# Performance work log

Measured on AMD Instinct MI355X. Metric: run time of the kernel, lower is better.

## Reference

```python
import jax, jax.numpy as jnp
import numpy as np

SPARSE_DEGREE = 4   # MUL_LEV_SPA_ATN_SPARSE_DEGREES[level=1]
NUM_HEADS = 16


def setup_inputs() -> dict:
    key = jax.random.key(0)
    k1, k2, k3 = jax.random.split(key, 3)
    S, B, H, Dh = 4096, 2, NUM_HEADS, 128  # [seq, batch, heads, head_dim]
    q = jax.random.normal(k1, (S, B, H, Dh), jnp.float32)
    k = jax.random.normal(k2, (S, B, H, Dh), jnp.float32)
    v = jax.random.normal(k3, (S, B, H, Dh), jnp.float32)
    return {"q": q, "k": k, "v": v}


def reference(q, k, v):
    # Single-device (world_size=1) MLSAForOneLevel forward, is_prompt=True.
    d = SPARSE_DEGREE
    S, B, H, Dh = q.shape
    Ssp = S // d  # number of sparse tokens per head

    # Per-head strided indices: head h selects tokens h%d, h%d+d, ...  -> [Ssp, H]
    idx = (jnp.arange(H) % d)[None, :] + d * jnp.arange(Ssp)[:, None]
    idx4 = jnp.broadcast_to(idx[:, None, :, None], (Ssp, B, H, Dh))
    gather0 = lambda x: jnp.take_along_axis(x, idx4, axis=0)
    q_ = gather0(q)  # prompt phase: q is also sparsified
    k_ = gather0(k)
    v_ = gather0(v)

    # Core attention (causal), layout [t, b, h, d]
    scale = 1.0 / jnp.sqrt(jnp.asarray(Dh, q.dtype))
    scores = jnp.einsum('tbhd,sbhd->bhts', q_, k_) * scale  # [B,H,Ssp,Ssp]
    causal = jnp.tril(jnp.ones((Ssp, Ssp), bool))
    scores = jnp.where(causal[None, None], scores, -jnp.inf)
    m = jnp.max(scores, axis=-1, keepdims=True)
    e = jnp.exp(scores - m)
    denom = jnp.sum(e, axis=-1, keepdims=True)          # softmax denominator [B,H,Ssp,1]
    probs = e / denom
    ctx = jnp.einsum('bhts,sbhd->tbhd', probs, v_)       # [Ssp,B,H,Dh]

    # Reconstruction scatter: rc_indices[token, h] = i where token = i*d + h%d, else Ssp (-> zero row)
    rc = jnp.full((S, H), Ssp, jnp.int32)
    rc = rc.at[idx, jnp.arange(H)[None, :]].set(jnp.arange(Ssp, dtype=jnp.int32)[:, None])
    padded = jnp.concatenate([ctx, jnp.zeros((1, B, H, Dh), ctx.dtype)], axis=0)
    rc4 = jnp.broadcast_to(rc[:, None, :, None], (S, B, H, Dh))
    out = jnp.take_along_axis(padded, rc4, axis=0)       # [S,B,H,Dh]

    denomi = jnp.transpose(denom, (2, 0, 1, 3)).astype(jnp.float32)  # 'b h t x -> t b h x'
    return out, denomi
```

## Files before the change

kernel.cpp:

```cpp
#include <hip/hip_runtime.h>
#include <hip/hip_bf16.h>

typedef __attribute__((ext_vector_type(8))) __bf16 bf16x8;
typedef __attribute__((ext_vector_type(4))) float f32x4;

#define S_TOK 4096
#define NB 2
#define NH 16
#define DH 128
#define DEG 4
#define SSP 1024
#define QB 64
#define KB 64
#define TOKS (NB * NH * DH)
#define SCALE 0.08838834764831845f
#define VP 148
#define KSZ (KB * 256)
#define VSZ (64 * VP)
#define BUFSZ (KSZ + VSZ)

union U8 {
  bf16x8 v;
  unsigned u[4];
  unsigned short s[8];
};

__device__ __forceinline__ unsigned short f2bfu(float x) {
  __bf16 b = (__bf16)x;
  return __builtin_bit_cast(unsigned short, b);
}
__device__ __forceinline__ unsigned pkbf(float lo, float hi) {
  return (unsigned)f2bfu(lo) | ((unsigned)f2bfu(hi) << 16);
}

__global__ __launch_bounds__(256, 2) void mlsa_fused(
    const float* __restrict__ Qg, const float* __restrict__ Kg,
    const float* __restrict__ Vg, float* __restrict__ Og,
    float* __restrict__ Dg) {
  __shared__ __align__(16) char lds[2 * BUFSZ];

  const int bid = blockIdx.x;
  const int bh = bid & 31;
  const int j = (bid >> 5) & 7;
  const int dhv = bid >> 8;
  const int b = bh >> 4;
  const int h = bh & 15;
  const int hm4 = h & 3;
  const int tid = (int)threadIdx.x;
  const int wv = tid >> 6;
  const int ln = tid & 63;
  const int g = ln >> 4;
  const int c = ln & 15;
  const size_t bhoff = (size_t)b * (NH * DH) + (size_t)h * DH;
  const int dbase = dhv * 64;

  const int krow = tid >> 2;
  const int kd0 = (tid & 3) * 8;
  const int vd4 = tid & 15;
  const int vsp = tid >> 4;

  f32x4 kreg[8], vreg[4];
  auto issue_kv = [&](int kt) {
    const float* kr =
        Kg + (size_t)((kt * KB + krow) * DEG + hm4) * TOKS + bhoff + kd0;
    #pragma unroll
    for (int p4 = 0; p4 < 4; ++p4) {
      kreg[2 * p4] = *(const f32x4*)(kr + p4 * 32);
      kreg[2 * p4 + 1] = *(const f32x4*)(kr + p4 * 32 + 4);
    }
    #pragma unroll
    for (int pp = 0; pp < 2; ++pp) {
      int s = kt * KB + pp * 32 + vsp * 2;
      const float* vr =
          Vg + (size_t)(s * DEG + hm4) * TOKS + bhoff + dbase + vd4 * 4;
      vreg[2 * pp] = *(const f32x4*)vr;
      vreg[2 * pp + 1] = *(const f32x4*)(vr + (size_t)DEG * TOKS);
    }
  };

  U8 kpk[4];
  unsigned vpk[2][4];
  auto conv = [&]() {
    #pragma unroll
    for (int p4 = 0; p4 < 4; ++p4) {
      #pragma unroll
      for (int i = 0; i < 4; ++i) {
        kpk[p4].s[i] = f2bfu(kreg[2 * p4][i]);
        kpk[p4].s[4 + i] = f2bfu(kreg[2 * p4 + 1][i]);
      }
    }
    #pragma unroll
    for (int pp = 0; pp < 2; ++pp) {
      #pragma unroll
      for (int jj = 0; jj < 4; ++jj)
        vpk[pp][jj] = pkbf(vreg[2 * pp][jj], vreg[2 * pp + 1][jj]);
    }
  };
  auto wr = [&](int buf) {
    char* KL = lds + buf * BUFSZ;
    char* VT = KL + KSZ;
    #pragma unroll
    for (int p4 = 0; p4 < 4; ++p4) {
      int d = kd0 + p4 * 32;
      int byte = (krow * 256 + d * 2) ^ ((krow & 7) << 4);
      *(bf16x8*)(KL + byte) = kpk[p4].v;
    }
    #pragma unroll
    for (int pp = 0; pp < 2; ++pp) {
      int s2 = (pp * 32 + vsp * 2) * 2;
      #pragma unroll
      for (int jj = 0; jj < 4; ++jj)
        *(unsigned*)(VT + (vd4 * 4 + jj) * VP + s2) = vpk[pp][jj];
    }
  };

  int cur = 0;

  for (int ph = 0; ph < 2; ++ph) {
    const int qt = ph ? (15 - j) : j;
    const int qbase = qt * QB + wv * 16;
    const int q_sp = qbase + c;

    f32x4 qraw[8];
    {
      const float* qrow =
          Qg + (size_t)(q_sp * DEG + hm4) * TOKS + bhoff + g * 8;
      #pragma unroll
      for (int dc = 0; dc < 4; ++dc) {
        qraw[2 * dc] = *(const f32x4*)(qrow + dc * 32);
        qraw[2 * dc + 1] = *(const f32x4*)(qrow + dc * 32 + 4);
      }
    }

    if (ph == 0) {
      issue_kv(0);
      const f32x4 z = {0.f, 0.f, 0.f, 0.f};
      for (int u = 0; u < 24; ++u) {
        int fid = u * 256 + tid;
        int col = fid & 15;
        int row = fid >> 4;
        int t2 = row >= 192;
        int r2 = row - (t2 ? 192 : 0);
        int rr = r2 >> 6;
        int qi = (t2 ? (15 - j) : j) * QB + (r2 & 63);
        int off = (hm4 + 1 + rr) & 3;
        *(f32x4*)(Og + (size_t)(qi * DEG + off) * TOKS + bhoff + dbase +
                  col * 4) = z;
      }
    }

    bf16x8 qf[4];
    #pragma unroll
    for (int dc = 0; dc < 4; ++dc) {
      U8 t;
      #pragma unroll
      for (int i = 0; i < 4; ++i) {
        t.s[i] = f2bfu(qraw[2 * dc][i] * SCALE);
        t.s[4 + i] = f2bfu(qraw[2 * dc + 1][i] * SCALE);
      }
      qf[dc] = t.v;
    }

    if (ph == 0) {
      conv();
      wr(0);
      __syncthreads();
      cur = 0;
    }

    float m_run = -1e30f, m_true = -1e30f, l_run = 0.f;
    f32x4 acc[4];
    #pragma unroll
    for (int i = 0; i < 4; ++i) acc[i] = (f32x4){0.f, 0.f, 0.f, 0.f};

    for (int kt = 0; kt <= qt; ++kt) {
      const bool diag = (kt == qt);
      const bool has_next = (kt < qt) || (ph == 0);
      if (has_next) {
        issue_kv(diag ? 0 : kt + 1);
        __builtin_amdgcn_sched_barrier(0);
      }

      const char* KL = lds + cur * BUFSZ;
      const char* VT = KL + KSZ;

      const int cbmax = diag ? wv : 3;
      f32x4 sc[4];
      #pragma unroll
      for (int cb = 0; cb < 4; ++cb) sc[cb] = (f32x4){0.f, 0.f, 0.f, 0.f};
      #pragma unroll
      for (int cb = 0; cb < 4; ++cb) {
        if (cb <= cbmax) {
          int rbase = (cb * 16 + c) * 256;
          int sw = (c & 7) << 4;
          #pragma unroll
          for (int dc = 0; dc < 4; ++dc) {
            int byte = (rbase + (dc * 32 + g * 8) * 2) ^ sw;
            bf16x8 kf = *(const bf16x8*)(KL + byte);
            sc[cb] =
                __builtin_amdgcn_mfma_f32_16x16x32_bf16(kf, qf[dc], sc[cb], 0, 0, 0);
          }
        }
      }

      float p[4][4];
      float mt = -1e30f;
      if (!diag) {
        #pragma unroll
        for (int cb = 0; cb < 4; ++cb) {
          #pragma unroll
          for (int r = 0; r < 4; ++r) {
            float v = sc[cb][r];
            p[cb][r] = v;
            mt = fmaxf(mt, v);
          }
        }
      } else {
        const int qloc = wv * 16 + c;
        #pragma unroll
        for (int cb = 0; cb < 4; ++cb) {
          #pragma unroll
          for (int r = 0; r < 4; ++r) {
            int kloc = cb * 16 + g * 4 + r;
            float v = (cb <= cbmax && kloc <= qloc) ? sc[cb][r] : -1e30f;
            p[cb][r] = v;
            mt = fmaxf(mt, v);
          }
        }
      }
      mt = fmaxf(mt, __shfl_xor(mt, 16));
      mt = fmaxf(mt, __shfl_xor(mt, 32));
      m_true = fmaxf(m_true, mt);

      float resc = 1.0f;
      if (!__all(mt <= m_run + 8.0f)) {
        float m_new = fmaxf(m_run, mt);
        resc = __expf(m_run - m_new);
        m_run = m_new;
        #pragma unroll
        for (int r = 0; r < 4; ++r) {
          float f = __shfl(resc, g * 4 + r);
          #pragma unroll
          for (int db = 0; db < 4; ++db) acc[db][r] *= f;
        }
      }
      float ls = 0.f;
      #pragma unroll
      for (int cb = 0; cb < 4; ++cb) {
        #pragma unroll
        for (int r = 0; r < 4; ++r) {
          float e = __expf(p[cb][r] - m_run);
          p[cb][r] = e;
          ls += e;
        }
      }
      ls += __shfl_xor(ls, 16);
      ls += __shfl_xor(ls, 32);
      l_run = l_run * resc + ls;

      unsigned pk2[4][2];
      #pragma unroll
      for (int cb = 0; cb < 4; ++cb) {
        pk2[cb][0] = pkbf(p[cb][0], p[cb][1]);
        pk2[cb][1] = pkbf(p[cb][2], p[cb][3]);
      }
      const int srcA = c + 16 * ((2 * g) & 3);
      const int srcB = c + 16 * ((2 * g + 1) & 3);
      const bool hi = (g & 2) != 0;

      if (has_next) conv();

      const int sbmax = diag ? (wv >> 1) : 1;
      #pragma unroll
      for (int sb = 0; sb < 2; ++sb) {
        if (sb <= sbmax) {
          unsigned a0 = (unsigned)__shfl((int)pk2[2 * sb][0], srcA);
          unsigned b0 = (unsigned)__shfl((int)pk2[2 * sb + 1][0], srcA);
          unsigned a1 = (unsigned)__shfl((int)pk2[2 * sb][1], srcA);
          unsigned b1 = (unsigned)__shfl((int)pk2[2 * sb + 1][1], srcA);
          unsigned a2 = (unsigned)__shfl((int)pk2[2 * sb][0], srcB);
          unsigned b2 = (unsigned)__shfl((int)pk2[2 * sb + 1][0], srcB);
          unsigned a3 = (unsigned)__shfl((int)pk2[2 * sb][1], srcB);
          unsigned b3 = (unsigned)__shfl((int)pk2[2 * sb + 1][1], srcB);
          U8 pa;
          pa.u[0] = hi ? b0 : a0;
          pa.u[1] = hi ? b1 : a1;
          pa.u[2] = hi ? b2 : a2;
          pa.u[3] = hi ? b3 : a3;
          #pragma unroll
          for (int db = 0; db < 4; ++db) {
            int byte = (db * 16 + c) * VP + (sb * 32 + g * 8) * 2;
            U8 vb;
            vb.u[0] = *(const unsigned*)(VT + byte);
            vb.u[1] = *(const unsigned*)(VT + byte + 4);
            vb.u[2] = *(const unsigned*)(VT + byte + 8);
            vb.u[3] = *(const unsigned*)(VT + byte + 12);
            acc[db] =
                __builtin_amdgcn_mfma_f32_16x16x32_bf16(pa.v, vb.v, acc[db], 0, 0, 0);
          }
        }
      }

      if (has_next) {
        wr(cur ^ 1);
        __syncthreads();
      }
      cur ^= 1;
    }

    float inv = 1.0f / l_run;
    #pragma unroll
    for (int r = 0; r < 4; ++r) {
      float fi = __shfl(inv, g * 4 + r);
      int q2 = qbase + g * 4 + r;
      float* orow = Og + (size_t)(q2 * DEG + hm4) * TOKS + bhoff + dbase;
      #pragma unroll
      for (int db = 0; db < 4; ++db) orow[db * 16 + c] = acc[db][r] * fi;
    }
    if (g == 0 && dhv == 0)
      Dg[(size_t)(qbase + c) * (NB * NH) + b * NH + h] =
          l_run * __expf(m_run - m_true);
  }
}

extern "C" void kernel_launch(void* const* d_in, const int* in_sizes, int n_in,
                              void* d_out, int out_size, void* d_ws, size_t ws_size,
                              hipStream_t stream) {
  (void)in_sizes; (void)n_in; (void)out_size; (void)d_ws; (void)ws_size;
  const float* q = (const float*)d_in[0];
  const float* k = (const float*)d_in[1];
  const float* v = (const float*)d_in[2];
  float* out = (float*)d_out;
  float* den = out + (size_t)S_TOK * NB * NH * DH;
  mlsa_fused<<<dim3(512), dim3(256), 0, stream>>>(q, k, v, out, den);
}
```

Measured before the change: 209.9 us.

## Pre-convert K/V to swizzled bf16 workspace and stage via direct global-to-LDS loads

```diff
diff --git a/kernel.cpp b/kernel.cpp
--- a/kernel.cpp
+++ b/kernel.cpp
@@ -12,12 +12,15 @@
 #define SSP 1024
 #define QB 64
 #define KB 64
-#define TOKS (NB * NH * DH)
+#define TOKS 4096
 #define SCALE 0.08838834764831845f
-#define VP 148
-#define KSZ (KB * 256)
-#define VSZ (64 * VP)
-#define BUFSZ (KSZ + VSZ)
+
+#define KROWB 256
+#define VROWB 2048
+#define KTILE (KB * KROWB)
+#define VTILE (64 * 128)
+#define BUFSZ (KTILE + VTILE)
+#define KB_BYTES (32L * 1024 * 256)
 
 union U8 {
   bf16x8 v;
@@ -32,14 +35,71 @@
 __device__ __forceinline__ unsigned pkbf(float lo, float hi) {
   return (unsigned)f2bfu(lo) | ((unsigned)f2bfu(hi) << 16);
 }
-
-__global__ __launch_bounds__(256, 2) void mlsa_fused(
-    const float* __restrict__ Qg, const float* __restrict__ Kg,
-    const float* __restrict__ Vg, float* __restrict__ Og,
+__device__ __forceinline__ void gload16(const void* g, void* l) {
+  __builtin_amdgcn_global_load_lds(
+      (const __attribute__((address_space(1))) unsigned*)g,
+      (__attribute__((address_space(3))) unsigned*)l, 16, 0, 0);
+}
+
+__global__ __launch_bounds__(256) void mlsa_conv(
+    const float* __restrict__ Kg, const float* __restrict__ Vg,
+    unsigned char* __restrict__ Kb, unsigned char* __restrict__ Vb) {
+  __shared__ __align__(16) unsigned char sm[64 * 144];
+  const int tid = (int)threadIdx.x;
+  const int bid = (int)blockIdx.x;
+  if (bid < 2048) {
+    int gid = bid * 256 + tid;
+    int row = gid >> 4;
+    int chunk = gid & 15;
+    int bh = row >> 10, s = row & 1023;
+    int b = bh >> 4, h = bh & 15;
+    long src = (long)(s * DEG + (h & 3)) * TOKS + b * (NH * DH) + h * DH + chunk * 8;
+    f32x4 x0 = *(const f32x4*)(Kg + src);
+    f32x4 x1 = *(const f32x4*)(Kg + src + 4);
+    uint4 w;
+    w.x = pkbf(x0[0], x0[1]);
+    w.y = pkbf(x0[2], x0[3]);
+    w.z = pkbf(x1[0], x1[1]);
+    w.w = pkbf(x1[2], x1[3]);
+    int col = (chunk * 16) ^ ((s & 7) << 4);
+    *(uint4*)(Kb + (long)row * KROWB + col) = w;
+  } else {
+    int vb = bid - 2048;
+    int bh = vb >> 5, st = (vb >> 1) & 15, dt = vb & 1;
+    int b = bh >> 4, h = bh & 15;
+    const int sl = (tid & 31) * 2;
+    const int dl = (tid >> 5) * 8;
+    long base = (long)((st * 64 + sl) * DEG + (h & 3)) * TOKS + b * (NH * DH) +
+                h * DH + dt * 64 + dl;
+    f32x4 a0 = *(const f32x4*)(Vg + base);
+    f32x4 a1 = *(const f32x4*)(Vg + base + 4);
+    f32x4 b0 = *(const f32x4*)(Vg + base + 4 * TOKS);
+    f32x4 b1 = *(const f32x4*)(Vg + base + 4 * TOKS + 4);
+    #pragma unroll
+    for (int i = 0; i < 4; ++i)
+      *(unsigned*)(sm + (dl + i) * 144 + sl * 2) = pkbf(a0[i], b0[i]);
+    #pragma unroll
+    for (int i = 0; i < 4; ++i)
+      *(unsigned*)(sm + (dl + 4 + i) * 144 + sl * 2) = pkbf(a1[i], b1[i]);
+    __syncthreads();
+    #pragma unroll
+    for (int rep = 0; rep < 2; ++rep) {
+      int id = tid + rep * 256;
+      int row = id >> 3, sc = id & 7;
+      uint4 w = *(const uint4*)(sm + row * 144 + sc * 16);
+      int colg = st * 128 + ((sc * 16) ^ ((row & 7) << 4));
+      *(uint4*)(Vb + ((long)bh * 128 + dt * 64 + row) * VROWB + colg) = w;
+    }
+  }
+}
+
+__global__ __launch_bounds__(256, 2) void mlsa_attn(
+    const float* __restrict__ Qg, const unsigned char* __restrict__ Kb,
+    const unsigned char* __restrict__ Vb, float* __restrict__ Og,
     float* __restrict__ Dg) {
-  __shared__ __align__(16) char lds[2 * BUFSZ];
-
-  const int bid = blockIdx.x;
+  __shared__ __align__(16) unsigned char lds[2 * BUFSZ];
+
+  const int bid = (int)blockIdx.x;
   const int bh = bid & 31;
   const int j = (bid >> 5) & 7;
   const int dhv = bid >> 8;
@@ -53,64 +113,24 @@
   const int c = ln & 15;
   const size_t bhoff = (size_t)b * (NH * DH) + (size_t)h * DH;
   const int dbase = dhv * 64;
-
-  const int krow = tid >> 2;
-  const int kd0 = (tid & 3) * 8;
-  const int vd4 = tid & 15;
-  const int vsp = tid >> 4;
-
-  f32x4 kreg[8], vreg[4];
-  auto issue_kv = [&](int kt) {
-    const float* kr =
-        Kg + (size_t)((kt * KB + krow) * DEG + hm4) * TOKS + bhoff + kd0;
-    #pragma unroll
-    for (int p4 = 0; p4 < 4; ++p4) {
-      kreg[2 * p4] = *(const f32x4*)(kr + p4 * 32);
-      kreg[2 * p4 + 1] = *(const f32x4*)(kr + p4 * 32 + 4);
-    }
-    #pragma unroll
-    for (int pp = 0; pp < 2; ++pp) {
-      int s = kt * KB + pp * 32 + vsp * 2;
-      const float* vr =
-          Vg + (size_t)(s * DEG + hm4) * TOKS + bhoff + dbase + vd4 * 4;
-      vreg[2 * pp] = *(const f32x4*)vr;
-      vreg[2 * pp + 1] = *(const f32x4*)(vr + (size_t)DEG * TOKS);
-    }
-  };
-
-  U8 kpk[4];
-  unsigned vpk[2][4];
-  auto conv = [&]() {
-    #pragma unroll
-    for (int p4 = 0; p4 < 4; ++p4) {
-      #pragma unroll
-      for (int i = 0; i < 4; ++i) {
-        kpk[p4].s[i] = f2bfu(kreg[2 * p4][i]);
-        kpk[p4].s[4 + i] = f2bfu(kreg[2 * p4 + 1][i]);
-      }
-    }
-    #pragma unroll
-    for (int pp = 0; pp < 2; ++pp) {
-      #pragma unroll
-      for (int jj = 0; jj < 4; ++jj)
-        vpk[pp][jj] = pkbf(vreg[2 * pp][jj], vreg[2 * pp + 1][jj]);
-    }
-  };
-  auto wr = [&](int buf) {
-    char* KL = lds + buf * BUFSZ;
-    char* VT = KL + KSZ;
-    #pragma unroll
-    for (int p4 = 0; p4 < 4; ++p4) {
-      int d = kd0 + p4 * 32;
-      int byte = (krow * 256 + d * 2) ^ ((krow & 7) << 4);
-      *(bf16x8*)(KL + byte) = kpk[p4].v;
-    }
-    #pragma unroll
-    for (int pp = 0; pp < 2; ++pp) {
-      int s2 = (pp * 32 + vsp * 2) * 2;
-      #pragma unroll
-      for (int jj = 0; jj < 4; ++jj)
-        *(unsigned*)(VT + (vd4 * 4 + jj) * VP + s2) = vpk[pp][jj];
+  const long kbase = (long)bh * (1024L * KROWB);
+  const long vbase = (long)bh * (128L * VROWB);
+
+  auto stage = [&](int buf, int kt) {
+    unsigned char* KL = lds + buf * BUFSZ;
+    unsigned char* VL = KL + KTILE;
+    #pragma unroll
+    for (int p = 0; p < 4; ++p) {
+      int off = wv * 4096 + p * 1024;
+      gload16(Kb + kbase + (long)kt * KTILE + off + ln * 16, KL + off);
+    }
+    #pragma unroll
+    for (int p = 0; p < 2; ++p) {
+      int off = wv * 2048 + p * 1024;
+      int o2 = off + ln * 16;
+      int row = o2 >> 7, colb = o2 & 127;
+      gload16(Vb + vbase + (long)(dbase + row) * VROWB + kt * 128 + colb,
+              VL + off);
     }
   };
 
@@ -121,10 +141,11 @@
     const int qbase = qt * QB + wv * 16;
     const int q_sp = qbase + c;
 
+    if (ph == 0) stage(0, 0);
+
     f32x4 qraw[8];
     {
-      const float* qrow =
-          Qg + (size_t)(q_sp * DEG + hm4) * TOKS + bhoff + g * 8;
+      const float* qrow = Qg + (size_t)(q_sp * DEG + hm4) * TOKS + bhoff + g * 8;
       #pragma unroll
       for (int dc = 0; dc < 4; ++dc) {
         qraw[2 * dc] = *(const f32x4*)(qrow + dc * 32);
@@ -133,7 +154,6 @@
     }
 
     if (ph == 0) {
-      issue_kv(0);
       const f32x4 z = {0.f, 0.f, 0.f, 0.f};
       for (int u = 0; u < 24; ++u) {
         int fid = u * 256 + tid;
@@ -144,8 +164,7 @@
         int rr = r2 >> 6;
         int qi = (t2 ? (15 - j) : j) * QB + (r2 & 63);
         int off = (hm4 + 1 + rr) & 3;
-        *(f32x4*)(Og + (size_t)(qi * DEG + off) * TOKS + bhoff + dbase +
-                  col * 4) = z;
+        *(f32x4*)(Og + (size_t)(qi * DEG + off) * TOKS + bhoff + dbase + col * 4) = z;
       }
     }
 
@@ -161,12 +180,7 @@
       qf[dc] = t.v;
     }
 
-    if (ph == 0) {
-      conv();
-      wr(0);
-      __syncthreads();
-      cur = 0;
-    }
+    if (ph == 0) __syncthreads();
 
     float m_run = -1e30f, m_true = -1e30f, l_run = 0.f;
     f32x4 acc[4];
@@ -177,12 +191,12 @@
       const bool diag = (kt == qt);
       const bool has_next = (kt < qt) || (ph == 0);
       if (has_next) {
-        issue_kv(diag ? 0 : kt + 1);
+        stage(cur ^ 1, diag ? 0 : kt + 1);
         __builtin_amdgcn_sched_barrier(0);
       }
 
-      const char* KL = lds + cur * BUFSZ;
-      const char* VT = KL + KSZ;
+      const unsigned char* KL = lds + cur * BUFSZ;
+      const unsigned char* VT = KL + KTILE;
 
       const int cbmax = diag ? wv : 3;
       f32x4 sc[4];
@@ -195,10 +209,9 @@
           int sw = (c & 7) << 4;
           #pragma unroll
           for (int dc = 0; dc < 4; ++dc) {
-            int byte = (rbase + (dc * 32 + g * 8) * 2) ^ sw;
+            int byte = rbase + ((dc * 64 + g * 16) ^ sw);
             bf16x8 kf = *(const bf16x8*)(KL + byte);
-            sc[cb] =
-                __builtin_amdgcn_mfma_f32_16x16x32_bf16(kf, qf[dc], sc[cb], 0, 0, 0);
+            sc[cb] = __builtin_amdgcn_mfma_f32_16x16x32_bf16(kf, qf[dc], sc[cb], 0, 0, 0);
           }
         }
       }
@@ -267,9 +280,6 @@
       const int srcA = c + 16 * ((2 * g) & 3);
       const int srcB = c + 16 * ((2 * g + 1) & 3);
       const bool hi = (g & 2) != 0;
-
-      if (has_next) conv();
-
       const int sbmax = diag ? (wv >> 1) : 1;
       #pragma unroll
       for (int sb = 0; sb < 2; ++sb) {
@@ -289,22 +299,16 @@
           pa.u[3] = hi ? b3 : a3;
           #pragma unroll
           for (int db = 0; db < 4; ++db) {
-            int byte = (db * 16 + c) * VP + (sb * 32 + g * 8) * 2;
-            U8 vb;
-            vb.u[0] = *(const unsigned*)(VT + byte);
-            vb.u[1] = *(const unsigned*)(VT + byte + 4);
-            vb.u[2] = *(const unsigned*)(VT + byte + 8);
-            vb.u[3] = *(const unsigned*)(VT + byte + 12);
-            acc[db] =
-                __builtin_amdgcn_mfma_f32_16x16x32_bf16(pa.v, vb.v, acc[db], 0, 0, 0);
+            int row = db * 16 + c;
+            int byte = row * 128 + (((sb * 32 + g * 8) * 2) ^ ((row & 7) << 4));
+            U8 vbf;
+            *(uint4*)vbf.u = *(const uint4*)(VT + byte);
+            acc[db] = __builtin_amdgcn_mfma_f32_16x16x32_bf16(pa.v, vbf.v, acc[db], 0, 0, 0);
           }
         }
       }
 
-      if (has_next) {
-        wr(cur ^ 1);
-        __syncthreads();
-      }
+      if (has_next) __syncthreads();
       cur ^= 1;
     }
 
@@ -326,11 +330,14 @@
 extern "C" void kernel_launch(void* const* d_in, const int* in_sizes, int n_in,
                               void* d_out, int out_size, void* d_ws, size_t ws_size,
                               hipStream_t stream) {
-  (void)in_sizes; (void)n_in; (void)out_size; (void)d_ws; (void)ws_size;
+  (void)in_sizes; (void)n_in; (void)out_size; (void)ws_size;
   const float* q = (const float*)d_in[0];
   const float* k = (const float*)d_in[1];
   const float* v = (const float*)d_in[2];
   float* out = (float*)d_out;
   float* den = out + (size_t)S_TOK * NB * NH * DH;
-  mlsa_fused<<<dim3(512), dim3(256), 0, stream>>>(q, k, v, out, den);
-}
+  unsigned char* Kb = (unsigned char*)d_ws;
+  unsigned char* Vb = Kb + KB_BYTES;
+  mlsa_conv<<<dim3(3072), dim3(256), 0, stream>>>(k, v, Kb, Vb);
+  mlsa_attn<<<dim3(512), dim3(256), 0, stream>>>(q, Kb, Vb, out, den);
+}
```

Result: no change. 213.8 us (+1.9%).
